# Performance work log

Hardware: AMD Instinct MI355X
Metric: run time of the kernel (lower is better)

## Reference

```python
import jax, jax.numpy as jnp
import numpy as np

B, S, H, NH = 2, 2048, 1024, 16
HD = H // NH  # 64
SCALE = HD ** -0.5


def setup_inputs() -> dict:
    key = jax.random.key(0)
    k1, k2, k3 = jax.random.split(key, 3)
    x = jax.random.normal(k1, (B, S, H), dtype=jnp.float32)
    w_qkv = jax.random.normal(k2, (H, 3 * H), dtype=jnp.float32) * (H ** -0.5)
    b_qkv = jnp.zeros((3 * H,), dtype=jnp.float32)
    w_out = jax.random.normal(k3, (H, H), dtype=jnp.float32) * (H ** -0.5)
    b_out = jnp.zeros((H,), dtype=jnp.float32)
    return {"x": x, "w_qkv": w_qkv, "b_qkv": b_qkv, "w_out": w_out, "b_out": b_out}


def reference(x, w_qkv, b_qkv, w_out, b_out):
    # qkv projection: [B,S,3H] -> split -> [B,NH,S,HD] each
    qkv = x @ w_qkv + b_qkv
    q, k, v = jnp.split(qkv, 3, axis=-1)
    def heads(t):
        return t.reshape(B, S, NH, HD).transpose(0, 2, 1, 3)  # [B,NH,S,HD]
    q, k, v = heads(q), heads(k), heads(v)
    # full (non-causal) softmax attention; chunking in the original is
    # math-equivalent since each query row attends over all keys
    scores = jnp.einsum('bhqd,bhkd->bhqk', q, k) * SCALE
    attn = jax.nn.softmax(scores, axis=-1)
    out = jnp.einsum('bhqk,bhkd->bhqd', attn, v)  # [B,NH,S,HD]
    out = out.transpose(0, 2, 1, 3).reshape(B, S, H)
    # to_out linear (Dropout is identity in eval mode)
    return out @ w_out + b_out
```

## Files before the change

### kernel.cpp

```cpp
#include <hip/hip_runtime.h>
#include <cstdint>

using u16 = unsigned short;
typedef __bf16 bf16x8 __attribute__((ext_vector_type(8)));
typedef __bf16 bf16x4 __attribute__((ext_vector_type(4)));
typedef __bf16 bf16x2 __attribute__((ext_vector_type(2)));
typedef float f32x4 __attribute__((ext_vector_type(4)));

#define MFMA16(a, b, c) __builtin_amdgcn_mfma_f32_16x16x32_bf16((a), (b), (c), 0, 0, 0)

__device__ __forceinline__ u16 f2bf(float f) {
  union { float f; uint32_t u; } c; c.f = f;
  uint32_t u = c.u;
  u += 0x7fffu + ((u >> 16) & 1u);
  return (u16)(u >> 16);
}

#if __has_builtin(__builtin_amdgcn_global_load_lds)
#define GLOAD_LDS16(g, l)                                                      \
  __builtin_amdgcn_global_load_lds(                                            \
      (__attribute__((address_space(1))) void*)(g),                            \
      (__attribute__((address_space(3))) void*)(l), 16, 0, 0)
#else
#define GLOAD_LDS16(g, l) do { *(uint4*)(l) = *(const uint4*)(g); } while (0)
#endif

__device__ __forceinline__ bf16x8 ptrans(const f32x4 lo, const f32x4 hi) {
  union W { bf16x2 h; uint32_t u; } wl0, wl1, wh0, wh1;
  wl0.h[0] = (__bf16)lo[0]; wl0.h[1] = (__bf16)lo[1];
  wl1.h[0] = (__bf16)lo[2]; wl1.h[1] = (__bf16)lo[3];
  wh0.h[0] = (__bf16)hi[0]; wh0.h[1] = (__bf16)hi[1];
  wh1.h[0] = (__bf16)hi[2]; wh1.h[1] = (__bf16)hi[3];
  uint32_t a0 = wl0.u, b0 = wh0.u, a1 = wl1.u, b1 = wh1.u;
  asm("v_permlane32_swap_b32 %0, %1" : "+v"(a0), "+v"(b0));
  asm("v_permlane16_swap_b32 %0, %1" : "+v"(a0), "+v"(b0));
  asm("v_permlane32_swap_b32 %0, %1" : "+v"(a1), "+v"(b1));
  asm("v_permlane16_swap_b32 %0, %1" : "+v"(a1), "+v"(b1));
  union R { uint32_t u[4]; bf16x8 v; } r;
  r.u[0] = a0; r.u[1] = a1; r.u[2] = b0; r.u[3] = b1;
  return r.v;
}

__global__ __launch_bounds__(256) void prep(
    const float* __restrict__ x, const float* __restrict__ w_qkv,
    const float* __restrict__ w_out, u16* __restrict__ xb,
    u16* __restrict__ wqT, u16* __restrict__ woT) {
  const int bid = blockIdx.x, tid = threadIdx.x;
  if (bid < 4096) {
    int i = (bid * 256 + tid) * 4;
    float4 v = *(const float4*)&x[i];
    ushort4 p;
    p.x = f2bf(v.x); p.y = f2bf(v.y); p.z = f2bf(v.z); p.w = f2bf(v.w);
    *(ushort4*)&xb[i] = p;
    return;
  }
  __shared__ float tile[32][33];
  int t = bid - 4096;
  const float* in;
  u16* outp;
  int C, bx, by;
  if (t < 3072) { in = w_qkv; outp = wqT; C = 3072; bx = (t % 96) * 32; by = (t / 96) * 32; }
  else { t -= 3072; in = w_out; outp = woT; C = 1024; bx = (t % 32) * 32; by = (t / 32) * 32; }
  const int tx = tid & 31, ty = tid >> 5;
#pragma unroll
  for (int r2 = 0; r2 < 4; ++r2)
    tile[ty + r2 * 8][tx] = in[(size_t)(by + ty + r2 * 8) * C + bx + tx];
  __syncthreads();
#pragma unroll
  for (int r2 = 0; r2 < 4; ++r2)
    outp[(size_t)(bx + ty + r2 * 8) * 1024 + by + tx] = f2bf(tile[tx][ty + r2 * 8]);
}

__global__ __launch_bounds__(256, 3) void gemm_qkv(
    const u16* __restrict__ A, const u16* __restrict__ Bt,
    const float* __restrict__ bias,
    u16* __restrict__ qb, u16* __restrict__ kb, u16* __restrict__ vb,
    int M, int N, int K) {
  __shared__ u16 As[128 * 32];
  __shared__ u16 Bs[128 * 32];
  const int tid = threadIdx.x;
  const int m0 = blockIdx.x * 128;
  const int n0 = blockIdx.y * 128;
  const int lane = tid & 63, w = tid >> 6;
  const int quad = lane >> 4, l16 = lane & 15;
  const int wr = w >> 1, wc = w & 1;

  f32x4 acc[4][4] = {};

  const int r0 = tid >> 2, p0 = tid & 3;
  const int r1 = r0 + 64;
  const int c8 = p0 ^ ((r0 >> 1) & 3);
  const u16* ga0 = A + (size_t)(m0 + r0) * K + c8 * 8;
  const u16* ga1 = A + (size_t)(m0 + r1) * K + c8 * 8;
  const u16* gb0 = Bt + (size_t)(n0 + r0) * K + c8 * 8;
  const u16* gb1 = Bt + (size_t)(n0 + r1) * K + c8 * 8;
  u16* la0 = &As[tid * 8];
  u16* la1 = &As[(tid + 256) * 8];
  u16* lb0 = &Bs[tid * 8];
  u16* lb1 = &Bs[(tid + 256) * 8];

  int aoff[4], boff[4];
#pragma unroll
  for (int i = 0; i < 4; ++i) {
    int ra = wr * 64 + i * 16 + l16;
    aoff[i] = (ra * 4 + (quad ^ ((ra >> 1) & 3))) * 8;
    int rb = wc * 64 + i * 16 + l16;
    boff[i] = (rb * 4 + (quad ^ ((rb >> 1) & 3))) * 8;
  }

  const int nIter = K >> 5;
  for (int kt = 0; kt < nIter; ++kt) {
    __syncthreads();
    const int kk = kt << 5;
    GLOAD_LDS16(ga0 + kk, la0);
    GLOAD_LDS16(ga1 + kk, la1);
    GLOAD_LDS16(gb0 + kk, lb0);
    GLOAD_LDS16(gb1 + kk, lb1);
    __syncthreads();
    bf16x8 af[4], bfr[4];
#pragma unroll
    for (int i = 0; i < 4; ++i) af[i] = *(const bf16x8*)&As[aoff[i]];
#pragma unroll
    for (int j = 0; j < 4; ++j) bfr[j] = *(const bf16x8*)&Bs[boff[j]];
#pragma unroll
    for (int i = 0; i < 4; ++i)
#pragma unroll
      for (int j = 0; j < 4; ++j)
        acc[i][j] = MFMA16(af[i], bfr[j], acc[i][j]);
  }

  const int S = 2048, NH = 16;
#pragma unroll
  for (int i = 0; i < 4; ++i) {
    const int mb = m0 + wr * 64 + i * 16 + quad * 4;
#pragma unroll
    for (int j = 0; j < 4; ++j) {
      const int n = n0 + wc * 64 + j * 16 + l16;
      const float bv = bias[n];
      const int which = n >> 10;
      const int hn = n & 1023;
      const int h = hn >> 6, d = hn & 63;
      const int b = mb >> 11, s = mb & 2047;
      const int bh = b * NH + h;
      if (which == 2) {
        ushort4 pk;
        pk.x = f2bf(acc[i][j][0] + bv);
        pk.y = f2bf(acc[i][j][1] + bv);
        pk.z = f2bf(acc[i][j][2] + bv);
        pk.w = f2bf(acc[i][j][3] + bv);
        *(ushort4*)&vb[((size_t)bh * 64 + d) * S + s] = pk;
      } else {
        const float sc = (which == 0) ? 0.18033688f : 1.0f;
        u16* dst = (which == 0) ? qb : kb;
#pragma unroll
        for (int r = 0; r < 4; ++r)
          dst[((size_t)bh * S + s + r) * 64 + d] = f2bf((acc[i][j][r] + bv) * sc);
      }
    }
  }
}

__global__ __launch_bounds__(256, 2) void gemm_out(
    const u16* __restrict__ A, const u16* __restrict__ Bt,
    const float* __restrict__ bias, float* __restrict__ outf,
    int M, int N, int K) {
  __shared__ u16 As[64 * 32];
  __shared__ u16 Bs[128 * 32];
  const int tid = threadIdx.x;
  const int m0 = blockIdx.x * 64;
  const int n0 = blockIdx.y * 128;
  const int lane = tid & 63, w = tid >> 6;
  const int quad = lane >> 4, l16 = lane & 15;
  const int wr = w >> 1, wc = w & 1;

  f32x4 acc[2][4] = {};

  const int r0 = tid >> 2, p0 = tid & 3;
  const int c8 = p0 ^ ((r0 >> 1) & 3);
  const u16* ga0 = A + (size_t)(m0 + r0) * K + c8 * 8;
  const u16* gb0 = Bt + (size_t)(n0 + r0) * K + c8 * 8;
  const u16* gb1 = Bt + (size_t)(n0 + r0 + 64) * K + c8 * 8;
  u16* la0 = &As[tid * 8];
  u16* lb0 = &Bs[tid * 8];
  u16* lb1 = &Bs[(tid + 256) * 8];

  int aoff[2], boff[4];
#pragma unroll
  for (int i = 0; i < 2; ++i) {
    int ra = wr * 32 + i * 16 + l16;
    aoff[i] = (ra * 4 + (quad ^ ((ra >> 1) & 3))) * 8;
  }
#pragma unroll
  for (int j = 0; j < 4; ++j) {
    int rb = wc * 64 + j * 16 + l16;
    boff[j] = (rb * 4 + (quad ^ ((rb >> 1) & 3))) * 8;
  }

  const int nIter = K >> 5;
  for (int kt = 0; kt < nIter; ++kt) {
    __syncthreads();
    const int kk = kt << 5;
    GLOAD_LDS16(ga0 + kk, la0);
    GLOAD_LDS16(gb0 + kk, lb0);
    GLOAD_LDS16(gb1 + kk, lb1);
    __syncthreads();
    bf16x8 af[2], bfr[4];
#pragma unroll
    for (int i = 0; i < 2; ++i) af[i] = *(const bf16x8*)&As[aoff[i]];
#pragma unroll
    for (int j = 0; j < 4; ++j) bfr[j] = *(const bf16x8*)&Bs[boff[j]];
#pragma unroll
    for (int i = 0; i < 2; ++i)
#pragma unroll
      for (int j = 0; j < 4; ++j)
        acc[i][j] = MFMA16(af[i], bfr[j], acc[i][j]);
  }

#pragma unroll
  for (int i = 0; i < 2; ++i) {
    const int mb = m0 + wr * 32 + i * 16 + quad * 4;
#pragma unroll
    for (int j = 0; j < 4; ++j) {
      const int n = n0 + wc * 64 + j * 16 + l16;
      const float bv = bias[n];
#pragma unroll
      for (int r = 0; r < 4; ++r)
        outf[(size_t)(mb + r) * N + n] = acc[i][j][r] + bv;
    }
  }
}

__global__ __launch_bounds__(256, 2) void attn_fa(
    const u16* __restrict__ qg, const u16* __restrict__ kg,
    const u16* __restrict__ vg, u16* __restrict__ o) {
  const int S = 2048;
  const int lin = blockIdx.x;
  const int xcd = lin & 7, chunk = lin >> 3;
  const int bh = xcd * 4 + (chunk & 3);
  const int qblk = chunk >> 2;
  const int b = bh >> 4, h = bh & 15;
  const int tid = threadIdx.x, w = tid >> 6, lane = tid & 63;
  const int quad = lane >> 4, l16 = lane & 15;

  __shared__ u16 Ks[2][8192];
  __shared__ u16 Vs[2][8192];

  const int q0 = qblk * 128 + w * 32;
  const u16* qp = qg + ((size_t)bh * S + q0 + l16) * 64 + quad * 8;
  const bf16x8 qf00 = *(const bf16x8*)qp;
  const bf16x8 qf01 = *(const bf16x8*)(qp + 32);
  const bf16x8 qf10 = *(const bf16x8*)(qp + 1024);
  const bf16x8 qf11 = *(const bf16x8*)(qp + 1024 + 32);

  f32x4 accO0[4] = {}, accO1[4] = {};
  f32x4 accL0 = {}, accL1 = {};

  bf16x8 ones;
#pragma unroll
  for (int i = 0; i < 8; ++i) ones[i] = (__bf16)1.0f;

  const u16* kbase = kg + (size_t)bh * S * 64;
  const u16* vbase = vg + (size_t)bh * 64 * S;

  const int sr0 = tid >> 3, sp0 = tid & 7;
  const int c8s = sp0 ^ (sr0 & 7);
  const u16* kSrc = kbase + (size_t)sr0 * 64 + c8s * 8;
  const int vr0 = tid >> 4, vp0 = tid & 15;
  const int vgs = vp0 ^ (vr0 & 7);
  const u16* vSrc = vbase + (size_t)vr0 * S + vgs * 8;

  const int kgA = (quad ^ (l16 & 7)) * 8;
  const int kgB = ((quad + 4) ^ (l16 & 7)) * 8;
  int vgA[2], vgB[2];
#pragma unroll
  for (int hh = 0; hh < 2; ++hh) {
    vgA[hh] = (hh * 8 + (quad ^ (l16 & 7))) * 8;
    vgB[hh] = (hh * 8 + ((quad + 4) ^ (l16 & 7))) * 8;
  }

#pragma unroll
  for (int seg = 0; seg < 4; ++seg) {
    GLOAD_LDS16(kSrc + (size_t)seg * 32 * 64, &Ks[0][(seg * 256 + tid) * 8]);
    GLOAD_LDS16(vSrc + (size_t)seg * 16 * S, &Vs[0][(seg * 256 + tid) * 8]);
  }

  for (int kt = 0; kt < 16; ++kt) {
    const int cur = kt & 1;
    __syncthreads();
    if (kt + 1 < 16) {
      const int nb = cur ^ 1;
#pragma unroll
      for (int seg = 0; seg < 4; ++seg) {
        GLOAD_LDS16(kSrc + (size_t)((kt + 1) * 128 + seg * 32) * 64,
                    &Ks[nb][(seg * 256 + tid) * 8]);
        GLOAD_LDS16(vSrc + (size_t)seg * 16 * S + (kt + 1) * 128,
                    &Vs[nb][(seg * 256 + tid) * 8]);
      }
    }
    const u16* Kc = Ks[cur];
    const u16* Vc = Vs[cur];

#pragma unroll
    for (int hh = 0; hh < 2; ++hh) {
      bf16x8 kf0[4], kf1[4];
#pragma unroll
      for (int ct = 0; ct < 4; ++ct) {
        const int rb = (hh * 64 + ct * 16 + l16) * 64;
        kf0[ct] = *(const bf16x8*)&Kc[rb + kgA];
        kf1[ct] = *(const bf16x8*)&Kc[rb + kgB];
      }
      f32x4 s0[4] = {}, s1[4] = {};
      __builtin_amdgcn_s_setprio(1);
#pragma unroll
      for (int ct = 0; ct < 4; ++ct) {
        s0[ct] = MFMA16(kf0[ct], qf00, s0[ct]);
        s0[ct] = MFMA16(kf1[ct], qf01, s0[ct]);
        s1[ct] = MFMA16(kf0[ct], qf10, s1[ct]);
        s1[ct] = MFMA16(kf1[ct], qf11, s1[ct]);
      }
      __builtin_amdgcn_s_setprio(0);

#pragma unroll
      for (int ct = 0; ct < 4; ++ct)
#pragma unroll
        for (int r = 0; r < 4; ++r) {
          s0[ct][r] = __builtin_amdgcn_exp2f(s0[ct][r]);
          s1[ct][r] = __builtin_amdgcn_exp2f(s1[ct][r]);
        }

      bf16x8 pf00 = ptrans(s0[0], s0[1]);
      bf16x8 pf01 = ptrans(s0[2], s0[3]);
      bf16x8 pf10 = ptrans(s1[0], s1[1]);
      bf16x8 pf11 = ptrans(s1[2], s1[3]);

      __builtin_amdgcn_s_setprio(1);
      accL0 = MFMA16(ones, pf00, accL0);
      accL0 = MFMA16(ones, pf01, accL0);
      accL1 = MFMA16(ones, pf10, accL1);
      accL1 = MFMA16(ones, pf11, accL1);

#pragma unroll
      for (int ct = 0; ct < 4; ++ct) {
        const int rb = (ct * 16 + l16) * 128;
        bf16x8 vf0 = *(const bf16x8*)&Vc[rb + vgA[hh]];
        bf16x8 vf1 = *(const bf16x8*)&Vc[rb + vgB[hh]];
        accO0[ct] = MFMA16(vf0, pf00, accO0[ct]);
        accO0[ct] = MFMA16(vf1, pf01, accO0[ct]);
        accO1[ct] = MFMA16(vf0, pf10, accO1[ct]);
        accO1[ct] = MFMA16(vf1, pf11, accO1[ct]);
      }
      __builtin_amdgcn_s_setprio(0);
    }
  }

  const float inv0 = 1.f / accL0[0], inv1 = 1.f / accL1[0];

  const int s0r = q0 + l16, s1r = q0 + 16 + l16;
#pragma unroll
  for (int ct = 0; ct < 4; ++ct) {
    ushort4 pk;
    pk.x = f2bf(accO0[ct][0] * inv0);
    pk.y = f2bf(accO0[ct][1] * inv0);
    pk.z = f2bf(accO0[ct][2] * inv0);
    pk.w = f2bf(accO0[ct][3] * inv0);
    *(ushort4*)&o[(size_t)(b * S + s0r) * 1024 + h * 64 + ct * 16 + quad * 4] = pk;
    pk.x = f2bf(accO1[ct][0] * inv1);
    pk.y = f2bf(accO1[ct][1] * inv1);
    pk.z = f2bf(accO1[ct][2] * inv1);
    pk.w = f2bf(accO1[ct][3] * inv1);
    *(ushort4*)&o[(size_t)(b * S + s1r) * 1024 + h * 64 + ct * 16 + quad * 4] = pk;
  }
}


extern "C" void kernel_launch(void* const* d_in, const int* in_sizes, int n_in,
                              void* d_out, int out_size, void* d_ws, size_t ws_size,
                              hipStream_t stream) {
  const float* x = (const float*)d_in[0];
  const float* w_qkv = (const float*)d_in[1];
  const float* b_qkv = (const float*)d_in[2];
  const float* w_out = (const float*)d_in[3];
  const float* b_out = (const float*)d_in[4];
  float* out = (float*)d_out;

  u16* xb = (u16*)d_ws;
  u16* wqT = xb + 4096 * 1024;
  u16* woT = wqT + 3072 * 1024;
  u16* qb = woT + 1024 * 1024;
  u16* kb = qb + 4194304;
  u16* vb = kb + 4194304;
  u16* ao = vb + 4194304;

  prep<<<8192, 256, 0, stream>>>(x, w_qkv, w_out, xb, wqT, woT);
  gemm_qkv<<<dim3(32, 24), 256, 0, stream>>>(xb, wqT, b_qkv, qb, kb, vb,
                                             4096, 3072, 1024);
  attn_fa<<<512, 256, 0, stream>>>(qb, kb, vb, ao);
  gemm_out<<<dim3(64, 8), 256, 0, stream>>>(ao, woT, b_out, out,
                                            4096, 1024, 1024);
}
```

Before: 175.6 us.

## Load V fragments directly from global memory instead of staging through LDS

V tiles are no longer double-buffered in shared memory. Each wave now reads its V MFMA operands straight from global memory (through the cache) at the start of each half-tile, and the V LDS buffers are removed. The smaller LDS footprint allows launch bounds to target three blocks per CU instead of two. The cost is redundant V global traffic across the four waves and load latency that is no longer hidden by the async double buffer, plus register pressure under the tighter occupancy bound.

```diff
diff --git a/kernel.cpp b/kernel.cpp
--- a/kernel.cpp
+++ b/kernel.cpp
@@ -230,7 +230,7 @@
   }
 }
 
-__global__ __launch_bounds__(256, 2) void attn_fa(
+__global__ __launch_bounds__(256, 3) void attn_fa(
     const u16* __restrict__ qg, const u16* __restrict__ kg,
     const u16* __restrict__ vg, u16* __restrict__ o) {
   const int S = 2048;
@@ -243,7 +243,6 @@
   const int quad = lane >> 4, l16 = lane & 15;
 
   __shared__ u16 Ks[2][8192];
-  __shared__ u16 Vs[2][8192];
 
   const int q0 = qblk * 128 + w * 32;
   const u16* qp = qg + ((size_t)bh * S + q0 + l16) * 64 + quad * 8;
@@ -265,24 +264,15 @@
   const int sr0 = tid >> 3, sp0 = tid & 7;
   const int c8s = sp0 ^ (sr0 & 7);
   const u16* kSrc = kbase + (size_t)sr0 * 64 + c8s * 8;
-  const int vr0 = tid >> 4, vp0 = tid & 15;
-  const int vgs = vp0 ^ (vr0 & 7);
-  const u16* vSrc = vbase + (size_t)vr0 * S + vgs * 8;
+
+  const u16* vB = vbase + (size_t)l16 * S + quad * 8;
 
   const int kgA = (quad ^ (l16 & 7)) * 8;
   const int kgB = ((quad + 4) ^ (l16 & 7)) * 8;
-  int vgA[2], vgB[2];
-#pragma unroll
-  for (int hh = 0; hh < 2; ++hh) {
-    vgA[hh] = (hh * 8 + (quad ^ (l16 & 7))) * 8;
-    vgB[hh] = (hh * 8 + ((quad + 4) ^ (l16 & 7))) * 8;
-  }
-
-#pragma unroll
-  for (int seg = 0; seg < 4; ++seg) {
+
+#pragma unroll
+  for (int seg = 0; seg < 4; ++seg)
     GLOAD_LDS16(kSrc + (size_t)seg * 32 * 64, &Ks[0][(seg * 256 + tid) * 8]);
-    GLOAD_LDS16(vSrc + (size_t)seg * 16 * S, &Vs[0][(seg * 256 + tid) * 8]);
-  }
 
   for (int kt = 0; kt < 16; ++kt) {
     const int cur = kt & 1;
@@ -290,18 +280,22 @@
     if (kt + 1 < 16) {
       const int nb = cur ^ 1;
 #pragma unroll
-      for (int seg = 0; seg < 4; ++seg) {
+      for (int seg = 0; seg < 4; ++seg)
         GLOAD_LDS16(kSrc + (size_t)((kt + 1) * 128 + seg * 32) * 64,
                     &Ks[nb][(seg * 256 + tid) * 8]);
-        GLOAD_LDS16(vSrc + (size_t)seg * 16 * S + (kt + 1) * 128,
-                    &Vs[nb][(seg * 256 + tid) * 8]);
-      }
     }
     const u16* Kc = Ks[cur];
-    const u16* Vc = Vs[cur];
 
 #pragma unroll
     for (int hh = 0; hh < 2; ++hh) {
+      bf16x8 vl0[4], vl1[4];
+      const size_t vcol = (size_t)(kt * 128 + hh * 64);
+#pragma unroll
+      for (int ct = 0; ct < 4; ++ct) {
+        vl0[ct] = *(const bf16x8*)&vB[(size_t)ct * 16 * S + vcol];
+        vl1[ct] = *(const bf16x8*)&vB[(size_t)ct * 16 * S + vcol + 32];
+      }
+
       bf16x8 kf0[4], kf1[4];
 #pragma unroll
       for (int ct = 0; ct < 4; ++ct) {
@@ -341,13 +335,10 @@
 
 #pragma unroll
       for (int ct = 0; ct < 4; ++ct) {
-        const int rb = (ct * 16 + l16) * 128;
-        bf16x8 vf0 = *(const bf16x8*)&Vc[rb + vgA[hh]];
-        bf16x8 vf1 = *(const bf16x8*)&Vc[rb + vgB[hh]];
-        accO0[ct] = MFMA16(vf0, pf00, accO0[ct]);
-        accO0[ct] = MFMA16(vf1, pf01, accO0[ct]);
-        accO1[ct] = MFMA16(vf0, pf10, accO1[ct]);
-        accO1[ct] = MFMA16(vf1, pf11, accO1[ct]);
+        accO0[ct] = MFMA16(vl0[ct], pf00, accO0[ct]);
+        accO0[ct] = MFMA16(vl1[ct], pf01, accO0[ct]);
+        accO1[ct] = MFMA16(vl0[ct], pf10, accO1[ct]);
+        accO1[ct] = MFMA16(vl1[ct], pf11, accO1[ct]);
       }
       __builtin_amdgcn_s_setprio(0);
     }
```

Result: slower. 201.6 us (+14.8%).

## Preload all K/V fragments per tile and merge half-tile passes in attention loop

Applied to the files above, without the earlier changes.

The V tile in shared memory is stored as two 64-key halves with 64-wide rows, using the same XOR swizzle as K, so V fragments use the same offsets as K. All K and V fragments for the 128-key tile are read from LDS right after the barrier and before the next tile's async global loads are issued. The two 64-key half passes are merged into one block of QK MFMAs, exp, and PV MFMAs, which gives the scheduler more independent work. The cost is higher register pressure from 32 preloaded fragments plus four score sets, which may reduce occupancy or cause spills.

```diff
diff --git a/kernel.cpp b/kernel.cpp
--- a/kernel.cpp
+++ b/kernel.cpp
@@ -265,92 +265,108 @@
   const int sr0 = tid >> 3, sp0 = tid & 7;
   const int c8s = sp0 ^ (sr0 & 7);
   const u16* kSrc = kbase + (size_t)sr0 * 64 + c8s * 8;
-  const int vr0 = tid >> 4, vp0 = tid & 15;
-  const int vgs = vp0 ^ (vr0 & 7);
-  const u16* vSrc = vbase + (size_t)vr0 * S + vgs * 8;
+  const int vd0 = tid >> 3, vg0 = tid & 7;
+  const u16* vSrc = vbase + (size_t)vd0 * S + (vg0 ^ (vd0 & 7)) * 8;
 
   const int kgA = (quad ^ (l16 & 7)) * 8;
   const int kgB = ((quad + 4) ^ (l16 & 7)) * 8;
-  int vgA[2], vgB[2];
-#pragma unroll
-  for (int hh = 0; hh < 2; ++hh) {
-    vgA[hh] = (hh * 8 + (quad ^ (l16 & 7))) * 8;
-    vgB[hh] = (hh * 8 + ((quad + 4) ^ (l16 & 7))) * 8;
-  }
 
 #pragma unroll
   for (int seg = 0; seg < 4; ++seg) {
     GLOAD_LDS16(kSrc + (size_t)seg * 32 * 64, &Ks[0][(seg * 256 + tid) * 8]);
-    GLOAD_LDS16(vSrc + (size_t)seg * 16 * S, &Vs[0][(seg * 256 + tid) * 8]);
+    GLOAD_LDS16(vSrc + (size_t)(seg & 1) * 32 * S + (seg >> 1) * 64,
+                &Vs[0][(seg * 256 + tid) * 8]);
   }
 
   for (int kt = 0; kt < 16; ++kt) {
     const int cur = kt & 1;
     __syncthreads();
+    const u16* Kc = Ks[cur];
+    const u16* Vc = Vs[cur];
+
+    bf16x8 kf00[4], kf01[4], kf10[4], kf11[4];
+    bf16x8 vf00[4], vf01[4], vf10[4], vf11[4];
+#pragma unroll
+    for (int ct = 0; ct < 4; ++ct) {
+      const int rb0 = (ct * 16 + l16) * 64;
+      const int rb1 = (64 + ct * 16 + l16) * 64;
+      kf00[ct] = *(const bf16x8*)&Kc[rb0 + kgA];
+      kf01[ct] = *(const bf16x8*)&Kc[rb0 + kgB];
+      kf10[ct] = *(const bf16x8*)&Kc[rb1 + kgA];
+      kf11[ct] = *(const bf16x8*)&Kc[rb1 + kgB];
+      vf00[ct] = *(const bf16x8*)&Vc[rb0 + kgA];
+      vf01[ct] = *(const bf16x8*)&Vc[rb0 + kgB];
+      vf10[ct] = *(const bf16x8*)&Vc[4096 + rb0 + kgA];
+      vf11[ct] = *(const bf16x8*)&Vc[4096 + rb0 + kgB];
+    }
+
     if (kt + 1 < 16) {
       const int nb = cur ^ 1;
 #pragma unroll
       for (int seg = 0; seg < 4; ++seg) {
         GLOAD_LDS16(kSrc + (size_t)((kt + 1) * 128 + seg * 32) * 64,
                     &Ks[nb][(seg * 256 + tid) * 8]);
-        GLOAD_LDS16(vSrc + (size_t)seg * 16 * S + (kt + 1) * 128,
+        GLOAD_LDS16(vSrc + (size_t)(seg & 1) * 32 * S + (kt + 1) * 128 +
+                        (seg >> 1) * 64,
                     &Vs[nb][(seg * 256 + tid) * 8]);
       }
     }
-    const u16* Kc = Ks[cur];
-    const u16* Vc = Vs[cur];
-
-#pragma unroll
-    for (int hh = 0; hh < 2; ++hh) {
-      bf16x8 kf0[4], kf1[4];
-#pragma unroll
-      for (int ct = 0; ct < 4; ++ct) {
-        const int rb = (hh * 64 + ct * 16 + l16) * 64;
-        kf0[ct] = *(const bf16x8*)&Kc[rb + kgA];
-        kf1[ct] = *(const bf16x8*)&Kc[rb + kgB];
+
+    f32x4 s0[4] = {}, s1[4] = {}, t0[4] = {}, t1[4] = {};
+    __builtin_amdgcn_s_setprio(1);
+#pragma unroll
+    for (int ct = 0; ct < 4; ++ct) {
+      s0[ct] = MFMA16(kf00[ct], qf00, s0[ct]);
+      s0[ct] = MFMA16(kf01[ct], qf01, s0[ct]);
+      s1[ct] = MFMA16(kf00[ct], qf10, s1[ct]);
+      s1[ct] = MFMA16(kf01[ct], qf11, s1[ct]);
+      t0[ct] = MFMA16(kf10[ct], qf00, t0[ct]);
+      t0[ct] = MFMA16(kf11[ct], qf01, t0[ct]);
+      t1[ct] = MFMA16(kf10[ct], qf10, t1[ct]);
+      t1[ct] = MFMA16(kf11[ct], qf11, t1[ct]);
+    }
+    __builtin_amdgcn_s_setprio(0);
+
+#pragma unroll
+    for (int ct = 0; ct < 4; ++ct)
+#pragma unroll
+      for (int r = 0; r < 4; ++r) {
+        s0[ct][r] = __builtin_amdgcn_exp2f(s0[ct][r]);
+        s1[ct][r] = __builtin_amdgcn_exp2f(s1[ct][r]);
+        t0[ct][r] = __builtin_amdgcn_exp2f(t0[ct][r]);
+        t1[ct][r] = __builtin_amdgcn_exp2f(t1[ct][r]);
       }
-      f32x4 s0[4] = {}, s1[4] = {};
-      __builtin_amdgcn_s_setprio(1);
-#pragma unroll
-      for (int ct = 0; ct < 4; ++ct) {
-        s0[ct] = MFMA16(kf0[ct], qf00, s0[ct]);
-        s0[ct] = MFMA16(kf1[ct], qf01, s0[ct]);
-        s1[ct] = MFMA16(kf0[ct], qf10, s1[ct]);
-        s1[ct] = MFMA16(kf1[ct], qf11, s1[ct]);
-      }
-      __builtin_amdgcn_s_setprio(0);
-
-#pragma unroll
-      for (int ct = 0; ct < 4; ++ct)
-#pragma unroll
-        for (int r = 0; r < 4; ++r) {
-          s0[ct][r] = __builtin_amdgcn_exp2f(s0[ct][r]);
-          s1[ct][r] = __builtin_amdgcn_exp2f(s1[ct][r]);
-        }
-
-      bf16x8 pf00 = ptrans(s0[0], s0[1]);
-      bf16x8 pf01 = ptrans(s0[2], s0[3]);
-      bf16x8 pf10 = ptrans(s1[0], s1[1]);
-      bf16x8 pf11 = ptrans(s1[2], s1[3]);
-
-      __builtin_amdgcn_s_setprio(1);
-      accL0 = MFMA16(ones, pf00, accL0);
-      accL0 = MFMA16(ones, pf01, accL0);
-      accL1 = MFMA16(ones, pf10, accL1);
-      accL1 = MFMA16(ones, pf11, accL1);
-
-#pragma unroll
-      for (int ct = 0; ct < 4; ++ct) {
-        const int rb = (ct * 16 + l16) * 128;
-        bf16x8 vf0 = *(const bf16x8*)&Vc[rb + vgA[hh]];
-        bf16x8 vf1 = *(const bf16x8*)&Vc[rb + vgB[hh]];
-        accO0[ct] = MFMA16(vf0, pf00, accO0[ct]);
-        accO0[ct] = MFMA16(vf1, pf01, accO0[ct]);
-        accO1[ct] = MFMA16(vf0, pf10, accO1[ct]);
-        accO1[ct] = MFMA16(vf1, pf11, accO1[ct]);
-      }
-      __builtin_amdgcn_s_setprio(0);
-    }
+
+    bf16x8 pf00 = ptrans(s0[0], s0[1]);
+    bf16x8 pf01 = ptrans(s0[2], s0[3]);
+    bf16x8 pf10 = ptrans(s1[0], s1[1]);
+    bf16x8 pf11 = ptrans(s1[2], s1[3]);
+    bf16x8 pg00 = ptrans(t0[0], t0[1]);
+    bf16x8 pg01 = ptrans(t0[2], t0[3]);
+    bf16x8 pg10 = ptrans(t1[0], t1[1]);
+    bf16x8 pg11 = ptrans(t1[2], t1[3]);
+
+    __builtin_amdgcn_s_setprio(1);
+    accL0 = MFMA16(ones, pf00, accL0);
+    accL0 = MFMA16(ones, pf01, accL0);
+    accL1 = MFMA16(ones, pf10, accL1);
+    accL1 = MFMA16(ones, pf11, accL1);
+    accL0 = MFMA16(ones, pg00, accL0);
+    accL0 = MFMA16(ones, pg01, accL0);
+    accL1 = MFMA16(ones, pg10, accL1);
+    accL1 = MFMA16(ones, pg11, accL1);
+#pragma unroll
+    for (int ct = 0; ct < 4; ++ct) {
+      accO0[ct] = MFMA16(vf00[ct], pf00, accO0[ct]);
+      accO0[ct] = MFMA16(vf01[ct], pf01, accO0[ct]);
+      accO1[ct] = MFMA16(vf00[ct], pf10, accO1[ct]);
+      accO1[ct] = MFMA16(vf01[ct], pf11, accO1[ct]);
+      accO0[ct] = MFMA16(vf10[ct], pg00, accO0[ct]);
+      accO0[ct] = MFMA16(vf11[ct], pg01, accO0[ct]);
+      accO1[ct] = MFMA16(vf10[ct], pg10, accO1[ct]);
+      accO1[ct] = MFMA16(vf11[ct], pg11, accO1[ct]);
+    }
+    __builtin_amdgcn_s_setprio(0);
   }
 
   const float inv0 = 1.f / accL0[0], inv1 = 1.f / accL1[0];
```

Result: no change. 172.7 us (-1.6%).
